# Performance work log

Hardware: AMD Instinct MI355X
Metric: run time of the kernel (lower is better)

## Reference

```python
import jax, jax.numpy as jnp
import numpy as np

NBINS = 15


def setup_inputs() -> dict:
    key = jax.random.key(0)
    k1, k2 = jax.random.split(key)
    N, C = 262144, 1000
    logits = jax.random.normal(k1, (N, C), dtype=jnp.float32)
    labels = jax.random.randint(k2, (N,), 0, C, dtype=jnp.int32)
    return {"logits": logits, "labels": labels}


def reference(logits, labels):
    N = logits.shape[0]
    probs = jax.nn.softmax(logits, axis=1)
    confidences = jnp.max(probs, axis=1)              # [N]
    predictions = jnp.argmax(probs, axis=1)           # [N]
    accuracies = (predictions == labels).astype(jnp.float32)

    # Equal-count (quantile) bin edges: np.interp(linspace(0,N,nbins+1), arange(N), sort(conf))
    conf_c = jax.lax.stop_gradient(confidences)
    sorted_conf = jnp.sort(conf_c)
    edges = jnp.interp(
        jnp.linspace(0.0, float(N), NBINS + 1),
        jnp.arange(N, dtype=jnp.float32),
        sorted_conf,
    )  # [NBINS+1]

    # torch semantics: bin i contains conf in (edges[i], edges[i+1]]
    bin_id = jnp.searchsorted(edges[1:], conf_c, side="left")   # [N] in [0, NBINS-1]
    bin_id = jnp.clip(bin_id, 0, NBINS - 1)
    # samples with conf <= edges[0] (== min) fall in no bin in the torch code
    valid = conf_c > edges[0]
    bin_id = jnp.where(valid, bin_id, NBINS)  # route invalid to an extra dump segment

    ones = jnp.ones((N,), dtype=jnp.float32)
    counts = jax.ops.segment_sum(ones, bin_id, num_segments=NBINS + 1)[:NBINS]
    sum_acc = jax.ops.segment_sum(accuracies, bin_id, num_segments=NBINS + 1)[:NBINS]
    sum_conf = jax.ops.segment_sum(confidences, bin_id, num_segments=NBINS + 1)[:NBINS]

    nonempty = counts > 0
    denom = jnp.maximum(counts, 1.0)
    avg_acc = sum_acc / denom
    avg_conf = sum_conf / denom
    prop_in_bin = counts / float(N)
    ece = jnp.sum(jnp.where(nonempty, jnp.abs(avg_conf - avg_acc) * prop_in_bin, 0.0))
    return ece.reshape(1)
```

## Files before the change

kernel.cpp:

```cpp
#include <hip/hip_runtime.h>
#include <math.h>

#define NBINS 15

__device__ __forceinline__ void rank_pair(int k, int N, int* i0, int* i1, double* frac) {
    double p = (double)k * (double)N / 15.0;
    double fl = floor(p);
    int a = (int)fl; if (a > N - 1) a = N - 1;
    int b = a + 1;   if (b > N - 1) b = N - 1;
    *i0 = a; *i1 = b; *frac = p - fl;
}

__global__ __launch_bounds__(256) void k_rowstats(
    const float* __restrict__ logits, const int* __restrict__ labels,
    float* __restrict__ conf, float* __restrict__ acc,
    unsigned int* __restrict__ hist1, int N, int C) {
    const int wid  = threadIdx.x >> 6;
    const int lane = threadIdx.x & 63;
    const int row  = blockIdx.x * 4 + wid;
    if (row >= N) return;

    const float*  rp = logits + (size_t)row * (size_t)C;
    const float4* rv = (const float4*)rp;
    const int nvec = C >> 2;

    float m = -INFINITY;
    float s = 0.0f;
    int   mi = 0;

    for (int k = lane; k < nvec; k += 64) {
        float4 v = rv[k];
        int idx = k << 2;
        { float x = v.x; float nm = fmaxf(m, x); s = s * __expf(m - nm) + __expf(x - nm); mi = (x > m) ? idx     : mi; m = nm; }
        { float x = v.y; float nm = fmaxf(m, x); s = s * __expf(m - nm) + __expf(x - nm); mi = (x > m) ? idx + 1 : mi; m = nm; }
        { float x = v.z; float nm = fmaxf(m, x); s = s * __expf(m - nm) + __expf(x - nm); mi = (x > m) ? idx + 2 : mi; m = nm; }
        { float x = v.w; float nm = fmaxf(m, x); s = s * __expf(m - nm) + __expf(x - nm); mi = (x > m) ? idx + 3 : mi; m = nm; }
    }
    for (int idx = (nvec << 2) + lane; idx < C; idx += 64) {
        float x = rp[idx]; float nm = fmaxf(m, x);
        s = s * __expf(m - nm) + __expf(x - nm);
        mi = (x > m) ? idx : mi; m = nm;
    }

    for (int off = 32; off > 0; off >>= 1) {
        float om  = __shfl_xor(m, off);
        float os  = __shfl_xor(s, off);
        int   omi = __shfl_xor(mi, off);
        float M = fmaxf(m, om);
        s = s * __expf(m - M) + os * __expf(om - M);
        if (om > m || (om == m && omi < mi)) mi = omi;
        m = M;
    }

    if (lane == 0) {
        float cv = 1.0f / s;
        conf[row] = cv;
        acc[row]  = (mi == labels[row]) ? 1.0f : 0.0f;
        atomicAdd(&hist1[__float_as_uint(cv) >> 16], 1u);
    }
}

__global__ void k_zero(unsigned int* p, int n) {
    int i = blockIdx.x * blockDim.x + threadIdx.x;
    if (i < n) p[i] = 0u;
}

__global__ __launch_bounds__(1024) void k_scan1(
    const unsigned int* __restrict__ hist1, unsigned int* __restrict__ meta, int N) {
    __shared__ unsigned int tmp[1024];
    __shared__ unsigned int R[32];
    const int t = threadIdx.x;
    if (t < 32) {
        int k = t >> 1; int i0, i1; double fr;
        rank_pair(k, N, &i0, &i1, &fr);
        R[t] = (unsigned int)((t & 1) ? i1 : i0);
    }
    const int base = t * 64;
    unsigned int local = 0;
    for (int b = 0; b < 64; b++) local += hist1[base + b];
    tmp[t] = local;
    __syncthreads();
    for (int off = 1; off < 1024; off <<= 1) {
        unsigned int v = (t >= off) ? tmp[t - off] : 0u;
        __syncthreads();
        tmp[t] += v;
        __syncthreads();
    }
    unsigned int cum = tmp[t] - local;
    for (int b = 0; b < 64; b++) {
        unsigned int c = hist1[base + b];
        if (c) {
            for (int j = 0; j < 32; j++) {
                unsigned int r = R[j];
                if (r >= cum && r < cum + c) {
                    meta[j]      = (unsigned int)(base + b);
                    meta[32 + j] = cum;
                }
            }
        }
        cum += c;
    }
}

__global__ __launch_bounds__(256) void k_hist2(
    const float* __restrict__ conf, const unsigned int* __restrict__ meta,
    unsigned int* __restrict__ hist2, int N) {
    __shared__ unsigned int bk[32];
    if (threadIdx.x < 32) bk[threadIdx.x] = meta[threadIdx.x];
    __syncthreads();
    int i = blockIdx.x * blockDim.x + threadIdx.x;
    if (i < N) {
        unsigned int key = __float_as_uint(conf[i]);
        unsigned int top = key >> 16, low = key & 0xFFFFu;
        #pragma unroll
        for (int j = 0; j < 32; j++)
            if (bk[j] == top) atomicAdd(&hist2[((unsigned int)j << 16) + low], 1u);
    }
}

__global__ __launch_bounds__(1024) void k_scan2(
    const unsigned int* __restrict__ hist2, unsigned int* __restrict__ meta, int N) {
    const int j = blockIdx.x;
    const unsigned int* h = hist2 + ((unsigned int)j << 16);
    __shared__ unsigned int tmp[1024];
    const int t = threadIdx.x;

    int k = j >> 1; int i0, i1; double fr;
    rank_pair(k, N, &i0, &i1, &fr);
    unsigned int target = (unsigned int)((j & 1) ? i1 : i0) - meta[32 + j];

    const int base = t * 64;
    unsigned int local = 0;
    for (int b = 0; b < 64; b++) local += h[base + b];
    tmp[t] = local;
    __syncthreads();
    for (int off = 1; off < 1024; off <<= 1) {
        unsigned int v = (t >= off) ? tmp[t - off] : 0u;
        __syncthreads();
        tmp[t] += v;
        __syncthreads();
    }
    unsigned int cum = tmp[t] - local;
    for (int b = 0; b < 64; b++) {
        unsigned int c = h[base + b];
        if (c && target >= cum && target < cum + c)
            meta[64 + j] = (meta[j] << 16) | (unsigned int)(base + b);
        cum += c;
    }
}

__global__ void k_edges(unsigned int* meta, int N) {
    int k = threadIdx.x;
    if (k >= 16) return;
    int i0, i1; double fr;
    rank_pair(k, N, &i0, &i1, &fr);
    float s0 = __uint_as_float(meta[64 + 2 * k]);
    float s1 = __uint_as_float(meta[64 + 2 * k + 1]);
    double e = (double)s0 + fr * ((double)s1 - (double)s0);
    ((double*)(meta + 96))[k] = e;
}

#define CNT_OFF  128
#define ACC_OFF  144
#define CONF_OFF 160

__global__ __launch_bounds__(256) void k_bin(
    const float* __restrict__ conf, const float* __restrict__ acc,
    float* __restrict__ metaf, int N) {
    __shared__ double e[16];
    __shared__ float c15[NBINS], a15[NBINS], f15[NBINS];
    const int t = threadIdx.x;
    if (t < 16) e[t] = ((const double*)(metaf + 96))[t];
    if (t < NBINS) { c15[t] = 0.f; a15[t] = 0.f; f15[t] = 0.f; }
    __syncthreads();
    int i = blockIdx.x * blockDim.x + t;
    if (i < N) {
        float cf = conf[i];
        double c = (double)cf;
        if (c > e[0]) {
            int bin = 0;
            #pragma unroll
            for (int k = 1; k < 16; k++) bin += (e[k] < c) ? 1 : 0;
            if (bin > NBINS - 1) bin = NBINS - 1;
            atomicAdd(&c15[bin], 1.0f);
            atomicAdd(&a15[bin], acc[i]);
            atomicAdd(&f15[bin], cf);
        }
    }
    __syncthreads();
    if (t < NBINS) {
        atomicAdd(&metaf[CNT_OFF + t],  c15[t]);
        atomicAdd(&metaf[ACC_OFF + t],  a15[t]);
        atomicAdd(&metaf[CONF_OFF + t], f15[t]);
    }
}

__global__ void k_final(const float* __restrict__ metaf, float* __restrict__ out, int N) {
    const int t = threadIdx.x;
    float term = 0.0f;
    if (t < NBINS) {
        float cnt = metaf[CNT_OFF + t];
        float sa  = metaf[ACC_OFF + t];
        float sc  = metaf[CONF_OFF + t];
        float denom = fmaxf(cnt, 1.0f);
        if (cnt > 0.0f) term = fabsf(sc / denom - sa / denom) * (cnt / (float)N);
    }
    for (int off = 32; off > 0; off >>= 1) term += __shfl_down(term, off);
    if (t == 0) out[0] = term;
}

extern "C" void kernel_launch(void* const* d_in, const int* in_sizes, int n_in,
                              void* d_out, int out_size, void* d_ws, size_t ws_size,
                              hipStream_t stream) {
    const float* logits = (const float*)d_in[0];
    const int*   labels = (const int*)d_in[1];
    const int N = in_sizes[1];
    const int C = in_sizes[0] / N;

    float* ws = (float*)d_ws;
    float*        conf  = ws;
    float*        acc   = ws + (size_t)N;
    unsigned int* hist1 = (unsigned int*)(ws + 2 * (size_t)N);
    unsigned int* meta  = hist1 + 65536;
    unsigned int* hist2 = meta + 256;
    float*        metaf = (float*)meta;
    float*        out   = (float*)d_out;

    const int nz = 65536 + 256 + 32 * 65536;
    k_zero<<<(nz + 255) / 256, 256, 0, stream>>>(hist1, nz);
    k_rowstats<<<(N + 3) / 4, 256, 0, stream>>>(logits, labels, conf, acc, hist1, N, C);
    k_scan1<<<1, 1024, 0, stream>>>(hist1, meta, N);
    k_hist2<<<(N + 255) / 256, 256, 0, stream>>>(conf, meta, hist2, N);
    k_scan2<<<32, 1024, 0, stream>>>(hist2, meta, N);
    k_edges<<<1, 64, 0, stream>>>(meta, N);
    k_bin<<<(N + 255) / 256, 256, 0, stream>>>(conf, acc, metaf, N);
    k_final<<<1, 64, 0, stream>>>(metaf, out, N);
}
```

Baseline: 648.3 us.

## Drop online softmax rescaling, fuse edge and final kernels into bin kernel

```diff
diff --git a/kernel.cpp b/kernel.cpp
--- a/kernel.cpp
+++ b/kernel.cpp
@@ -2,6 +2,11 @@
 #include <math.h>
 
 #define NBINS 15
+
+#define CNT_OFF   128
+#define ACC_OFF   144
+#define CONF_OFF  160
+#define TICKET_OFF 176
 
 __device__ __forceinline__ void rank_pair(int k, int N, int* i0, int* i1, double* frac) {
     double p = (double)k * (double)N / 15.0;
@@ -24,45 +29,49 @@
     const float4* rv = (const float4*)rp;
     const int nvec = C >> 2;
 
-    float m = -INFINITY;
-    float s = 0.0f;
-    int   mi = 0;
+    float m0 = -INFINITY, m1 = -INFINITY, m2 = -INFINITY, m3 = -INFINITY;
+    float s0 = 0.f, s1 = 0.f, s2 = 0.f, s3 = 0.f;
+    int   i0 = 0, i1 = 1, i2 = 2, i3 = 3;
 
     for (int k = lane; k < nvec; k += 64) {
         float4 v = rv[k];
         int idx = k << 2;
-        { float x = v.x; float nm = fmaxf(m, x); s = s * __expf(m - nm) + __expf(x - nm); mi = (x > m) ? idx     : mi; m = nm; }
-        { float x = v.y; float nm = fmaxf(m, x); s = s * __expf(m - nm) + __expf(x - nm); mi = (x > m) ? idx + 1 : mi; m = nm; }
-        { float x = v.z; float nm = fmaxf(m, x); s = s * __expf(m - nm) + __expf(x - nm); mi = (x > m) ? idx + 2 : mi; m = nm; }
-        { float x = v.w; float nm = fmaxf(m, x); s = s * __expf(m - nm) + __expf(x - nm); mi = (x > m) ? idx + 3 : mi; m = nm; }
+        s0 += __expf(v.x); if (v.x > m0) { m0 = v.x; i0 = idx;     }
+        s1 += __expf(v.y); if (v.y > m1) { m1 = v.y; i1 = idx + 1; }
+        s2 += __expf(v.z); if (v.z > m2) { m2 = v.z; i2 = idx + 2; }
+        s3 += __expf(v.w); if (v.w > m3) { m3 = v.w; i3 = idx + 3; }
     }
     for (int idx = (nvec << 2) + lane; idx < C; idx += 64) {
-        float x = rp[idx]; float nm = fmaxf(m, x);
-        s = s * __expf(m - nm) + __expf(x - nm);
-        mi = (x > m) ? idx : mi; m = nm;
-    }
+        float x = rp[idx];
+        s0 += __expf(x);
+        if (x > m0) { m0 = x; i0 = idx; }
+    }
+
+    float m = m0; int mi = i0;
+    if (m1 > m || (m1 == m && i1 < mi)) { m = m1; mi = i1; }
+    if (m2 > m || (m2 == m && i2 < mi)) { m = m2; mi = i2; }
+    if (m3 > m || (m3 == m && i3 < mi)) { m = m3; mi = i3; }
+    float s = (s0 + s1) + (s2 + s3);
 
     for (int off = 32; off > 0; off >>= 1) {
         float om  = __shfl_xor(m, off);
         float os  = __shfl_xor(s, off);
         int   omi = __shfl_xor(mi, off);
-        float M = fmaxf(m, om);
-        s = s * __expf(m - M) + os * __expf(om - M);
-        if (om > m || (om == m && omi < mi)) mi = omi;
-        m = M;
+        s += os;
+        if (om > m || (om == m && omi < mi)) { m = om; mi = omi; }
     }
 
     if (lane == 0) {
-        float cv = 1.0f / s;
+        float cv = __expf(m) / s;
         conf[row] = cv;
         acc[row]  = (mi == labels[row]) ? 1.0f : 0.0f;
         atomicAdd(&hist1[__float_as_uint(cv) >> 16], 1u);
     }
 }
 
-__global__ void k_zero(unsigned int* p, int n) {
+__global__ void k_zero4(uint4* p, int n4) {
     int i = blockIdx.x * blockDim.x + threadIdx.x;
-    if (i < n) p[i] = 0u;
+    if (i < n4) p[i] = make_uint4(0u, 0u, 0u, 0u);
 }
 
 __global__ __launch_bounds__(1024) void k_scan1(
@@ -71,9 +80,9 @@
     __shared__ unsigned int R[32];
     const int t = threadIdx.x;
     if (t < 32) {
-        int k = t >> 1; int i0, i1; double fr;
-        rank_pair(k, N, &i0, &i1, &fr);
-        R[t] = (unsigned int)((t & 1) ? i1 : i0);
+        int k = t >> 1; int a, b; double fr;
+        rank_pair(k, N, &a, &b, &fr);
+        R[t] = (unsigned int)((t & 1) ? b : a);
     }
     const int base = t * 64;
     unsigned int local = 0;
@@ -125,13 +134,13 @@
     __shared__ unsigned int tmp[1024];
     const int t = threadIdx.x;
 
-    int k = j >> 1; int i0, i1; double fr;
-    rank_pair(k, N, &i0, &i1, &fr);
-    unsigned int target = (unsigned int)((j & 1) ? i1 : i0) - meta[32 + j];
+    int k = j >> 1; int a, b; double fr;
+    rank_pair(k, N, &a, &b, &fr);
+    unsigned int target = (unsigned int)((j & 1) ? b : a) - meta[32 + j];
 
     const int base = t * 64;
     unsigned int local = 0;
-    for (int b = 0; b < 64; b++) local += h[base + b];
+    for (int bb = 0; bb < 64; bb++) local += h[base + bb];
     tmp[t] = local;
     __syncthreads();
     for (int off = 1; off < 1024; off <<= 1) {
@@ -141,38 +150,33 @@
         __syncthreads();
     }
     unsigned int cum = tmp[t] - local;
-    for (int b = 0; b < 64; b++) {
-        unsigned int c = h[base + b];
+    for (int bb = 0; bb < 64; bb++) {
+        unsigned int c = h[base + bb];
         if (c && target >= cum && target < cum + c)
-            meta[64 + j] = (meta[j] << 16) | (unsigned int)(base + b);
+            meta[64 + j] = (meta[j] << 16) | (unsigned int)(base + bb);
         cum += c;
     }
 }
-
-__global__ void k_edges(unsigned int* meta, int N) {
-    int k = threadIdx.x;
-    if (k >= 16) return;
-    int i0, i1; double fr;
-    rank_pair(k, N, &i0, &i1, &fr);
-    float s0 = __uint_as_float(meta[64 + 2 * k]);
-    float s1 = __uint_as_float(meta[64 + 2 * k + 1]);
-    double e = (double)s0 + fr * ((double)s1 - (double)s0);
-    ((double*)(meta + 96))[k] = e;
-}
-
-#define CNT_OFF  128
-#define ACC_OFF  144
-#define CONF_OFF 160
 
 __global__ __launch_bounds__(256) void k_bin(
     const float* __restrict__ conf, const float* __restrict__ acc,
-    float* __restrict__ metaf, int N) {
+    unsigned int* __restrict__ meta, float* __restrict__ out, int N) {
+    float* metaf = (float*)meta;
     __shared__ double e[16];
     __shared__ float c15[NBINS], a15[NBINS], f15[NBINS];
+    __shared__ unsigned int amLast;
     const int t = threadIdx.x;
-    if (t < 16) e[t] = ((const double*)(metaf + 96))[t];
+
+    if (t < 16) {
+        int a, b; double fr;
+        rank_pair(t, N, &a, &b, &fr);
+        float v0 = __uint_as_float(meta[64 + 2 * t]);
+        float v1 = __uint_as_float(meta[64 + 2 * t + 1]);
+        e[t] = (double)v0 + fr * ((double)v1 - (double)v0);
+    }
     if (t < NBINS) { c15[t] = 0.f; a15[t] = 0.f; f15[t] = 0.f; }
     __syncthreads();
+
     int i = blockIdx.x * blockDim.x + t;
     if (i < N) {
         float cf = conf[i];
@@ -193,20 +197,25 @@
         atomicAdd(&metaf[ACC_OFF + t],  a15[t]);
         atomicAdd(&metaf[CONF_OFF + t], f15[t]);
     }
-}
-
-__global__ void k_final(const float* __restrict__ metaf, float* __restrict__ out, int N) {
-    const int t = threadIdx.x;
-    float term = 0.0f;
-    if (t < NBINS) {
-        float cnt = metaf[CNT_OFF + t];
-        float sa  = metaf[ACC_OFF + t];
-        float sc  = metaf[CONF_OFF + t];
-        float denom = fmaxf(cnt, 1.0f);
-        if (cnt > 0.0f) term = fabsf(sc / denom - sa / denom) * (cnt / (float)N);
-    }
-    for (int off = 32; off > 0; off >>= 1) term += __shfl_down(term, off);
-    if (t == 0) out[0] = term;
+    __threadfence();
+    __syncthreads();
+    if (t == 0)
+        amLast = (atomicAdd(&meta[TICKET_OFF], 1u) == (unsigned int)(gridDim.x - 1)) ? 1u : 0u;
+    __syncthreads();
+
+    if (amLast) {
+        float term = 0.0f;
+        if (t < NBINS) {
+            float cnt = atomicAdd(&metaf[CNT_OFF + t],  0.0f);
+            float sa  = atomicAdd(&metaf[ACC_OFF + t],  0.0f);
+            float sc  = atomicAdd(&metaf[CONF_OFF + t], 0.0f);
+            if (cnt > 0.0f) term = fabsf(sc / cnt - sa / cnt) * (cnt / (float)N);
+        }
+        if (t < 64) {
+            for (int off = 32; off > 0; off >>= 1) term += __shfl_down(term, off);
+            if (t == 0) out[0] = term;
+        }
+    }
 }
 
 extern "C" void kernel_launch(void* const* d_in, const int* in_sizes, int n_in,
@@ -223,16 +232,14 @@
     unsigned int* hist1 = (unsigned int*)(ws + 2 * (size_t)N);
     unsigned int* meta  = hist1 + 65536;
     unsigned int* hist2 = meta + 256;
-    float*        metaf = (float*)meta;
     float*        out   = (float*)d_out;
 
-    const int nz = 65536 + 256 + 32 * 65536;
-    k_zero<<<(nz + 255) / 256, 256, 0, stream>>>(hist1, nz);
+    const int nz  = 65536 + 256 + 32 * 65536;
+    const int nz4 = nz / 4;
+    k_zero4<<<(nz4 + 255) / 256, 256, 0, stream>>>((uint4*)hist1, nz4);
     k_rowstats<<<(N + 3) / 4, 256, 0, stream>>>(logits, labels, conf, acc, hist1, N, C);
     k_scan1<<<1, 1024, 0, stream>>>(hist1, meta, N);
     k_hist2<<<(N + 255) / 256, 256, 0, stream>>>(conf, meta, hist2, N);
     k_scan2<<<32, 1024, 0, stream>>>(hist2, meta, N);
-    k_edges<<<1, 64, 0, stream>>>(meta, N);
-    k_bin<<<(N + 255) / 256, 256, 0, stream>>>(conf, acc, metaf, N);
-    k_final<<<1, 64, 0, stream>>>(metaf, out, N);
-}
+    k_bin<<<(N + 255) / 256, 256, 0, stream>>>(conf, acc, meta, out, N);
+}
```

Result: slower. 684.5 us (+5.6%).
